# Kernel optimization log

Hardware: AMD Instinct MI355X
Metric: run time of the kernel (lower is better)

The kernel has to match this reference:

```python
import jax, jax.numpy as jnp
import numpy as np

L, H, D, DH, F, V, S, B, CTX = 6, 12, 768, 64, 3072, 32000, 1024, 2, 1024
EPS = 1e-5


def layernorm(x, scale, bias):
    mu = jnp.mean(x, axis=-1, keepdims=True)
    var = jnp.mean(jnp.square(x - mu), axis=-1, keepdims=True)
    return (x - mu) * jax.lax.rsqrt(var + EPS) * scale + bias


def setup_inputs() -> dict:
    key = jax.random.key(0)
    ks = jax.random.split(key, 16)
    std = 0.02
    res_std = 0.02 * (2 * L) ** (-0.5)
    inp = {
        "X": jax.random.randint(ks[0], (B, S), 0, V),
        "emb": jax.random.normal(ks[1], (V, D), jnp.float32) * std,            # tied with head weight
        "pos_emb": jax.random.normal(ks[2], (CTX, D), jnp.float32) * 0.01,
        "Wq": jax.random.normal(ks[3], (L, H, D, DH), jnp.float32) * std,
        "bq": jnp.zeros((L, H, DH), jnp.float32),
        "Wk": jax.random.normal(ks[4], (L, H, D, DH), jnp.float32) * std,
        "bk": jnp.zeros((L, H, DH), jnp.float32),
        "Wv": jax.random.normal(ks[5], (L, H, D, DH), jnp.float32) * std,
        "bv": jnp.zeros((L, H, DH), jnp.float32),
        "Wo": jax.random.normal(ks[6], (L, H * DH, D), jnp.float32) * res_std,  # ResidualScaledLinear
        "bo": jnp.zeros((L, D), jnp.float32),
        "ln1_s": jnp.ones((L, D), jnp.float32),
        "ln1_b": jnp.zeros((L, D), jnp.float32),
        "ln2_s": jnp.ones((L, D), jnp.float32),
        "ln2_b": jnp.zeros((L, D), jnp.float32),
        "W1": jax.random.normal(ks[7], (L, D, F), jnp.float32) * std,
        "b1": jnp.zeros((L, F), jnp.float32),
        "W2": jax.random.normal(ks[8], (L, F, D), jnp.float32) * res_std,       # ResidualScaledLinear
        "b2": jnp.zeros((L, D), jnp.float32),
        "lnf_s": jnp.ones((D,), jnp.float32),
        "lnf_b": jnp.zeros((D,), jnp.float32),
        "head_b": jnp.zeros((V,), jnp.float32),
    }
    return inp


def decoder_forward(X, emb, pos_emb, Wq, bq, Wk, bk, Wv, bv, Wo, bo,
                    ln1_s, ln1_b, ln2_s, ln2_b, W1, b1, W2, b2,
                    lnf_s, lnf_b, head_b):
    seq = X.shape[1]
    x = emb[X] + pos_emb[:seq]                      # [B,S,D]
    causal = jnp.tril(jnp.ones((seq, seq), bool))   # tril mask buffer
    scale = 1.0 / jnp.sqrt(jnp.float32(DH))
    for l in range(L):
        xn = layernorm(x, ln1_s[l], ln1_b[l])
        q = jnp.einsum('bsd,hdk->bhsk', xn, Wq[l]) + bq[l][None, :, None, :]
        k = jnp.einsum('bsd,hdk->bhsk', xn, Wk[l]) + bk[l][None, :, None, :]
        v = jnp.einsum('bsd,hdk->bhsk', xn, Wv[l]) + bv[l][None, :, None, :]
        scores = jnp.einsum('bhsk,bhtk->bhst', q, k) * scale
        scores = jnp.where(causal, scores, -jnp.inf)
        attn = jax.nn.softmax(scores, axis=-1)
        out = jnp.einsum('bhst,bhtk->bshk', attn, v).reshape(x.shape[0], seq, H * DH)
        x = x + out @ Wo[l] + bo[l]
        xn2 = layernorm(x, ln2_s[l], ln2_b[l])
        x = x + jax.nn.relu(xn2 @ W1[l] + b1[l]) @ W2[l] + b2[l]
    x = layernorm(x, lnf_s, lnf_b)
    return x @ emb.T + head_b                       # tied head weight


def reference(X, emb, pos_emb, Wq, bq, Wk, bk, Wv, bv, Wo, bo,
              ln1_s, ln1_b, ln2_s, ln2_b, W1, b1, W2, b2,
              lnf_s, lnf_b, head_b):
    return decoder_forward(X, emb, pos_emb, Wq, bq, Wk, bk, Wv, bv, Wo, bo,
                           ln1_s, ln1_b, ln2_s, ln2_b, W1, b1, W2, b2,
                           lnf_s, lnf_b, head_b)
```

## Files before the change

kernel.cpp:

```cpp
#include <hip/hip_runtime.h>
#include <cstdint>
#include <cstddef>

#define CL 6
#define CH 12
#define CD 768
#define CDH 64
#define CF 3072
#define CV 32000
#define CS 1024
#define CB 2
#define CM (CB*CS)
#define CQS 2304

typedef unsigned short u16;
typedef __bf16 bf16x8 __attribute__((ext_vector_type(8)));
typedef float f32x4 __attribute__((ext_vector_type(4)));

__device__ __forceinline__ float bf2f(u16 u) {
  union { unsigned int i; float f; } c; c.i = ((unsigned int)u) << 16; return c.f;
}
__device__ __forceinline__ u16 f2bf(float f) {
  union { float f; unsigned int i; } c; c.f = f;
  unsigned int lsb = (c.i >> 16) & 1u;
  c.i += 0x7fffu + lsb;
  return (u16)(c.i >> 16);
}

__device__ __forceinline__ void gload16(const u16* g, u16* l) {
  __builtin_amdgcn_global_load_lds(
      (const __attribute__((address_space(1))) void*)g,
      (__attribute__((address_space(3))) void*)l, 16, 0, 0);
}

__global__ __launch_bounds__(256) void convert_kernel(
    const float* __restrict__ src, u16* __restrict__ dst, int total)
{
  int idx = blockIdx.x * 256 + threadIdx.x;
  if (idx < total) dst[idx] = f2bf(src[idx]);
}

__global__ __launch_bounds__(256) void embed_kernel(
    const int* __restrict__ X, const float* __restrict__ emb,
    const float* __restrict__ pos, float* __restrict__ x)
{
  int idx = blockIdx.x * 256 + threadIdx.x;
  int m = idx / CD, d = idx - m * CD;
  int s = m & (CS - 1);
  x[idx] = emb[(size_t)X[m] * CD + d] + pos[s * CD + d];
}

__global__ __launch_bounds__(256) void ln_kernel(
    const float* __restrict__ x, const float* __restrict__ gs,
    const float* __restrict__ gb, u16* __restrict__ out)
{
  __shared__ float rs[4], rss[4];
  int row = blockIdx.x, tid = threadIdx.x;
  const float* xr = x + (size_t)row * CD;
  float a0 = xr[tid], a1 = xr[tid + 256], a2 = xr[tid + 512];
  float s = a0 + a1 + a2;
  float ss = a0 * a0 + a1 * a1 + a2 * a2;
#pragma unroll
  for (int sh = 32; sh > 0; sh >>= 1) {
    s  += __shfl_xor(s, sh, 64);
    ss += __shfl_xor(ss, sh, 64);
  }
  int w = tid >> 6;
  if ((tid & 63) == 0) { rs[w] = s; rss[w] = ss; }
  __syncthreads();
  s  = rs[0] + rs[1] + rs[2] + rs[3];
  ss = rss[0] + rss[1] + rss[2] + rss[3];
  float mu = s * (1.f / CD);
  float inv = rsqrtf(ss * (1.f / CD) - mu * mu + 1e-5f);
  u16* orow = out + (size_t)row * CD;
  orow[tid]       = f2bf((a0 - mu) * inv * gs[tid]       + gb[tid]);
  orow[tid + 256] = f2bf((a1 - mu) * inv * gs[tid + 256] + gb[tid + 256]);
  orow[tid + 512] = f2bf((a2 - mu) * inv * gs[tid + 512] + gb[tid + 512]);
}

__global__ __launch_bounds__(256) void trans_kernel(
    u16* __restrict__ dst, const float* __restrict__ src, int R, int C,
    int PB, long dstL)
{
  __shared__ float st[32][65];
  int r0 = blockIdx.x * 64, c0 = blockIdx.y * 32, bz = blockIdx.z;
  const float* s = src + (size_t)bz * R * C;
  u16* d = dst + (size_t)(bz / PB) * dstL + (size_t)(bz % PB) * R * C;
  int tx = threadIdx.x & 31, ty = threadIdx.x >> 5;
#pragma unroll
  for (int i = 0; i < 8; i++) {
    int r = ty + 8 * i;
    st[tx][r] = s[(size_t)(r0 + r) * C + c0 + tx];
  }
  __syncthreads();
  int j = threadIdx.x & 15, cbase = threadIdx.x >> 4;
#pragma unroll
  for (int i = 0; i < 2; i++) {
    int c = cbase + 16 * i;
    uint2 pk;
    u16* p = (u16*)&pk;
    p[0] = f2bf(st[c][4 * j + 0]);
    p[1] = f2bf(st[c][4 * j + 1]);
    p[2] = f2bf(st[c][4 * j + 2]);
    p[3] = f2bf(st[c][4 * j + 3]);
    *(uint2*)&d[(size_t)(c0 + c) * R + r0 + 4 * j] = pk;
  }
}

__global__ __launch_bounds__(256) void biaspack_kernel(
    const float* __restrict__ bq, const float* __restrict__ bk,
    const float* __restrict__ bv, float* __restrict__ dst)
{
  int idx = blockIdx.x * 256 + threadIdx.x;
  int l = idx / CQS, c = idx - l * CQS;
  float val;
  if (c < 768)       val = bq[l * 768 + c];
  else if (c < 1536) val = bk[l * 768 + c - 768];
  else               val = bv[l * 768 + c - 1536];
  dst[idx] = val;
}

template<bool RES, bool RELU, bool OUTBF>
__global__ __launch_bounds__(256) void gemm64v2_kernel(
    const u16* __restrict__ A, const u16* __restrict__ Bt,
    const float* __restrict__ bias, const float* __restrict__ res,
    void* __restrict__ outp, int M, int N, int K)
{
  __shared__ __align__(16) u16 As[64 * 64];
  __shared__ __align__(16) u16 Bs[64 * 64];
  int tid = threadIdx.x;
  int m0 = blockIdx.y * 64, n0 = blockIdx.x * 64;
  int wv = tid >> 6, ln = tid & 63;
  int quad = ln >> 4, l16 = ln & 15;
  int wm = (wv >> 1) * 32, wn = (wv & 1) * 32;

  int srow = wv * 8 + (ln >> 3);
  int scol = (ln & 7) * 8;
  const u16* gA = A  + (size_t)(m0 + srow) * K + scol;
  const u16* gB = Bt + (size_t)(n0 + srow) * K + scol;

  f32x4 acc[2][2];
  acc[0][0] = f32x4{0,0,0,0}; acc[0][1] = f32x4{0,0,0,0};
  acc[1][0] = f32x4{0,0,0,0}; acc[1][1] = f32x4{0,0,0,0};

  for (int kt = 0; kt < K; kt += 64) {
    __syncthreads();
#pragma unroll
    for (int it = 0; it < 2; it++) {
      gload16(gA + (size_t)it * 32 * K + kt, As + it * 2048 + wv * 512);
      gload16(gB + (size_t)it * 32 * K + kt, Bs + it * 2048 + wv * 512);
    }
    __syncthreads();
#pragma unroll
    for (int h = 0; h < 2; h++) {
      bf16x8 af[2], bf[2];
#pragma unroll
      for (int i = 0; i < 2; i++) {
        af[i] = *reinterpret_cast<const bf16x8*>(&As[(wm + i * 16 + l16) * 64 + h * 32 + quad * 8]);
        bf[i] = *reinterpret_cast<const bf16x8*>(&Bs[(wn + i * 16 + l16) * 64 + h * 32 + quad * 8]);
      }
#pragma unroll
      for (int i = 0; i < 2; i++)
#pragma unroll
        for (int j = 0; j < 2; j++)
          acc[i][j] = __builtin_amdgcn_mfma_f32_16x16x32_bf16(af[i], bf[j], acc[i][j], 0, 0, 0);
    }
  }

#pragma unroll
  for (int i = 0; i < 2; i++) {
    int gmb = m0 + wm + i * 16 + quad * 4;
#pragma unroll
    for (int j = 0; j < 2; j++) {
      int gn = n0 + wn + j * 16 + l16;
      float bsv = bias[gn];
#pragma unroll
      for (int rr = 0; rr < 4; rr++) {
        float val = acc[i][j][rr] + bsv;
        if (RELU) val = fmaxf(val, 0.f);
        size_t o = (size_t)(gmb + rr) * N + gn;
        if (RES) val += res[o];
        if (OUTBF) ((u16*)outp)[o] = f2bf(val);
        else       ((float*)outp)[o] = val;
      }
    }
  }
}

template<bool RES, bool RELU, bool OUTBF>
__global__ __launch_bounds__(256) void gemm128_kernel(
    const u16* __restrict__ A, const u16* __restrict__ Bt,
    const float* __restrict__ bias, const float* __restrict__ res,
    void* __restrict__ outp, int M, int N, int K)
{
  __shared__ __align__(16) u16 As[128 * 64];
  __shared__ __align__(16) u16 Bs[128 * 64];
  int tid = threadIdx.x;
  int nbm = M >> 7, nbn = N >> 7, nwg = nbm * nbn;
  int orig = blockIdx.x;
  int q8 = nwg >> 3, r8 = nwg & 7;
  int xcd = orig & 7;
  int t = ((xcd < r8) ? xcd * (q8 + 1) : r8 * (q8 + 1) + (xcd - r8) * q8) + (orig >> 3);
  int bm = t % nbm, bn = t / nbm;
  int m0 = bm << 7, n0 = bn << 7;

  int wv = tid >> 6, ln = tid & 63;
  int quad = ln >> 4, l16 = ln & 15;
  int wr = wv >> 1, wc = wv & 1;

  int srow = wv * 8 + (ln >> 3);
  int scol = (ln & 7) * 8;
  const u16* gA = A  + (size_t)(m0 + srow) * K + scol;
  const u16* gB = Bt + (size_t)(n0 + srow) * K + scol;

  f32x4 acc[4][4];
#pragma unroll
  for (int i = 0; i < 4; i++)
#pragma unroll
    for (int j = 0; j < 4; j++) acc[i][j] = f32x4{0.f, 0.f, 0.f, 0.f};

  for (int kt = 0; kt < K; kt += 64) {
    __syncthreads();
#pragma unroll
    for (int it = 0; it < 4; it++) {
      gload16(gA + (size_t)it * 32 * K + kt, As + it * 2048 + wv * 512);
      gload16(gB + (size_t)it * 32 * K + kt, Bs + it * 2048 + wv * 512);
    }
    __syncthreads();
#pragma unroll
    for (int h = 0; h < 2; h++) {
      bf16x8 af[4], bf[4];
#pragma unroll
      for (int i = 0; i < 4; i++)
        af[i] = *reinterpret_cast<const bf16x8*>(&As[(wr * 64 + i * 16 + l16) * 64 + h * 32 + quad * 8]);
#pragma unroll
      for (int j = 0; j < 4; j++)
        bf[j] = *reinterpret_cast<const bf16x8*>(&Bs[(wc * 64 + j * 16 + l16) * 64 + h * 32 + quad * 8]);
#pragma unroll
      for (int i = 0; i < 4; i++)
#pragma unroll
        for (int j = 0; j < 4; j++)
          acc[i][j] = __builtin_amdgcn_mfma_f32_16x16x32_bf16(af[i], bf[j], acc[i][j], 0, 0, 0);
    }
  }

#pragma unroll
  for (int i = 0; i < 4; i++) {
    int gm = m0 + wr * 64 + i * 16 + quad * 4;
#pragma unroll
    for (int j = 0; j < 4; j++) {
      int gn = n0 + wc * 64 + j * 16 + l16;
      float bsv = bias[gn];
#pragma unroll
      for (int rr = 0; rr < 4; rr++) {
        float val = acc[i][j][rr] + bsv;
        if (RELU) val = fmaxf(val, 0.f);
        size_t oo = (size_t)(gm + rr) * N + gn;
        if (RES) val += res[oo];
        if (OUTBF) ((u16*)outp)[oo] = f2bf(val);
        else       ((float*)outp)[oo] = val;
      }
    }
  }
}

__global__ __launch_bounds__(256) void attn_mfma_kernel(
    const u16* __restrict__ qkv, u16* __restrict__ o)
{
  __shared__ __align__(16) u16 Ks[64 * 64];
  __shared__ __align__(16) u16 Vt[64 * 64];
  __shared__ __align__(16) u16 Ps[4 * 16 * 64];

  int tid = threadIdx.x;
  int qb = (CS / 64 - 1) - blockIdx.x;
  int h = blockIdx.y, b = blockIdx.z;
  int wid = tid >> 6, lane = tid & 63, quad = lane >> 4, l16 = lane & 15;
  int q0 = qb * 64;
  size_t bh = (size_t)b * CS * CQS + h * CDH;

  bf16x8 aq[2];
  {
    const u16* qrow = qkv + bh + (size_t)(q0 + wid * 16 + l16) * CQS;
#pragma unroll
    for (int ks = 0; ks < 2; ks++) {
      uint4 t = *(const uint4*)(qrow + ks * 32 + quad * 8);
      aq[ks] = *reinterpret_cast<bf16x8*>(&t);
    }
  }

  f32x4 oacc[4];
  float mrow[4], lrow[4];
#pragma unroll
  for (int j = 0; j < 4; j++) oacc[j] = f32x4{0.f, 0.f, 0.f, 0.f};
#pragma unroll
  for (int r = 0; r < 4; r++) { mrow[r] = -1e30f; lrow[r] = 0.f; }

  int srow = tid >> 3, schunk = tid & 7;
  int vrow = tid >> 2, vseg = (tid & 3) * 16;

  for (int t0 = 0; t0 <= q0; t0 += 64) {
    __syncthreads();
#pragma unroll
    for (int it = 0; it < 2; it++) {
      int row = srow + it * 32;
      uint4 kv4 = *(const uint4*)(qkv + bh + 768 + (size_t)(t0 + row) * CQS + schunk * 8);
      *(uint4*)&Ks[row * 64 + ((schunk ^ (row & 7)) * 8)] = kv4;
    }
    {
      const u16* vr = qkv + bh + 1536 + (size_t)(t0 + vrow) * CQS + vseg;
      uint4 a0 = *(const uint4*)(vr);
      uint4 a1 = *(const uint4*)(vr + 8);
      int c = vrow >> 3, w7 = vrow & 7;
#pragma unroll
      for (int i = 0; i < 16; i++) {
        int d = vseg + i;
        u16 val = (i < 8) ? ((const u16*)&a0)[i] : ((const u16*)&a1)[i - 8];
        Vt[d * 64 + (((c ^ (d & 7)) * 8) | w7)] = val;
      }
    }
    __syncthreads();

    f32x4 sacc[4];
#pragma unroll
    for (int j = 0; j < 4; j++) sacc[j] = f32x4{0.f, 0.f, 0.f, 0.f};
#pragma unroll
    for (int j = 0; j < 4; j++) {
      int row = j * 16 + l16;
#pragma unroll
      for (int ks = 0; ks < 2; ks++) {
        bf16x8 bk = *reinterpret_cast<const bf16x8*>(
            &Ks[row * 64 + ((((ks * 4 + quad) ^ (row & 7)) * 8))]);
        sacc[j] = __builtin_amdgcn_mfma_f32_16x16x32_bf16(aq[ks], bk, sacc[j], 0, 0, 0);
      }
    }

    int qg0 = q0 + wid * 16 + quad * 4;
#pragma unroll
    for (int j = 0; j < 4; j++) {
      int tg = t0 + j * 16 + l16;
#pragma unroll
      for (int r = 0; r < 4; r++) {
        float s = sacc[j][r] * 0.125f;
        sacc[j][r] = (tg <= qg0 + r) ? s : -1e30f;
      }
    }

#pragma unroll
    for (int r = 0; r < 4; r++) {
      float m = fmaxf(fmaxf(sacc[0][r], sacc[1][r]), fmaxf(sacc[2][r], sacc[3][r]));
#pragma unroll
      for (int sh = 1; sh < 16; sh <<= 1) m = fmaxf(m, __shfl_xor(m, sh, 64));
      float mnew = fmaxf(mrow[r], m);
      float scal = __expf(mrow[r] - mnew);
      mrow[r] = mnew;
      lrow[r] *= scal;
#pragma unroll
      for (int j = 0; j < 4; j++) oacc[j][r] *= scal;
      float sum = 0.f;
#pragma unroll
      for (int j = 0; j < 4; j++) {
        float p = __expf(sacc[j][r] - mnew);
        sacc[j][r] = p;
        sum += p;
      }
#pragma unroll
      for (int sh = 1; sh < 16; sh <<= 1) sum += __shfl_xor(sum, sh, 64);
      lrow[r] += sum;
    }

    u16* Pw = Ps + wid * 1024;
#pragma unroll
    for (int j = 0; j < 4; j++) {
      int c = (l16 >> 3) + 2 * j;
#pragma unroll
      for (int r = 0; r < 4; r++) {
        int row = quad * 4 + r;
        Pw[row * 64 + (((c ^ (row & 7)) * 8) | (l16 & 7))] = f2bf(sacc[j][r]);
      }
    }

    bf16x8 ap[2];
#pragma unroll
    for (int ks = 0; ks < 2; ks++)
      ap[ks] = *reinterpret_cast<const bf16x8*>(
          &Pw[l16 * 64 + ((((ks * 4 + quad) ^ (l16 & 7)) * 8))]);
#pragma unroll
    for (int j = 0; j < 4; j++) {
      int row = j * 16 + l16;
#pragma unroll
      for (int ks = 0; ks < 2; ks++) {
        bf16x8 bv = *reinterpret_cast<const bf16x8*>(
            &Vt[row * 64 + ((((ks * 4 + quad) ^ (row & 7)) * 8))]);
        oacc[j] = __builtin_amdgcn_mfma_f32_16x16x32_bf16(ap[ks], bv, oacc[j], 0, 0, 0);
      }
    }
  }

#pragma unroll
  for (int r = 0; r < 4; r++) {
    float inv = 1.f / lrow[r];
    int qg = q0 + wid * 16 + quad * 4 + r;
    u16* orow = o + (size_t)b * CS * CD + h * CDH + (size_t)qg * CD;
#pragma unroll
    for (int j = 0; j < 4; j++)
      orow[j * 16 + l16] = f2bf(oacc[j][r] * inv);
  }
}

extern "C" void kernel_launch(void* const* d_in, const int* in_sizes, int n_in,
                              void* d_out, int out_size, void* d_ws, size_t ws_size,
                              hipStream_t stream) {
  const int*   X      = (const int*)d_in[0];
  const float* emb    = (const float*)d_in[1];
  const float* pos    = (const float*)d_in[2];
  const float* Wq     = (const float*)d_in[3];
  const float* bq     = (const float*)d_in[4];
  const float* Wk     = (const float*)d_in[5];
  const float* bk     = (const float*)d_in[6];
  const float* Wv     = (const float*)d_in[7];
  const float* bv     = (const float*)d_in[8];
  const float* Wo     = (const float*)d_in[9];
  const float* bo     = (const float*)d_in[10];
  const float* ln1s   = (const float*)d_in[11];
  const float* ln1b   = (const float*)d_in[12];
  const float* ln2s   = (const float*)d_in[13];
  const float* ln2b   = (const float*)d_in[14];
  const float* W1     = (const float*)d_in[15];
  const float* b1     = (const float*)d_in[16];
  const float* W2     = (const float*)d_in[17];
  const float* b2     = (const float*)d_in[18];
  const float* lnfs   = (const float*)d_in[19];
  const float* lnfb   = (const float*)d_in[20];
  const float* headb  = (const float*)d_in[21];
  (void)in_sizes; (void)n_in; (void)out_size;

  char* ws = (char*)d_ws;
  size_t off = 0;
  auto alloc = [&](size_t bytes) { void* p = ws + off; off += (bytes + 255) & ~(size_t)255; return p; };

  float* x     = (float*)alloc((size_t)CM * CD * 4);
  u16*   xn    = (u16*)  alloc((size_t)CM * CD * 2);
  u16*   qkvb  = (u16*)  alloc((size_t)CM * CQS * 2);
  u16*   ao    = (u16*)  alloc((size_t)CM * CD * 2);
  u16*   hb    = (u16*)  alloc((size_t)CM * CF * 2);
  u16*   embC  = (u16*)  alloc((size_t)CV * CD * 2);
  float* biasp = (float*)alloc((size_t)CL * CQS * 4);

  const size_t WQKV = (size_t)CQS * CD;
  const size_t WOO  = (size_t)CD * CD;
  const size_t WFF  = (size_t)CD * CF;
  size_t perLayerElems = WQKV + WOO + 2 * WFF;
  bool fused = (ws_size >= off + (size_t)CL * perLayerElems * 2 + 4096);
  int LW = fused ? CL : 1;
  u16* Wqkvt = (u16*)alloc((size_t)LW * WQKV * 2);
  u16* Wot   = (u16*)alloc((size_t)LW * WOO * 2);
  u16* W1t   = (u16*)alloc((size_t)LW * WFF * 2);
  u16* W2t   = (u16*)alloc((size_t)LW * WFF * 2);

  embed_kernel<<<CM * CD / 256, 256, 0, stream>>>(X, emb, pos, x);
  convert_kernel<<<(CV * CD) / 256, 256, 0, stream>>>(emb, embC, CV * CD);
  biaspack_kernel<<<(CL * CQS) / 256, 256, 0, stream>>>(bq, bk, bv, biasp);

  if (fused) {
    trans_kernel<<<dim3(CD / 64, CDH / 32, CL * CH), 256, 0, stream>>>(Wqkvt,              Wq, CD, CDH, CH, (long)WQKV);
    trans_kernel<<<dim3(CD / 64, CDH / 32, CL * CH), 256, 0, stream>>>(Wqkvt + 768 * 768,  Wk, CD, CDH, CH, (long)WQKV);
    trans_kernel<<<dim3(CD / 64, CDH / 32, CL * CH), 256, 0, stream>>>(Wqkvt + 1536 * 768, Wv, CD, CDH, CH, (long)WQKV);
    trans_kernel<<<dim3(CD / 64, CD / 32, CL), 256, 0, stream>>>(Wot, Wo, CD, CD, 1, (long)WOO);
    trans_kernel<<<dim3(CD / 64, CF / 32, CL), 256, 0, stream>>>(W1t, W1, CD, CF, 1, (long)WFF);
    trans_kernel<<<dim3(CF / 64, CD / 32, CL), 256, 0, stream>>>(W2t, W2, CF, CD, 1, (long)WFF);
  }

  const int QKV_TOT = CH * CD * CDH;

  for (int l = 0; l < CL; l++) {
    if (!fused) {
      trans_kernel<<<dim3(CD / 64, CDH / 32, CH), 256, 0, stream>>>(Wqkvt,              Wq + (size_t)l * QKV_TOT, CD, CDH, CH, (long)WQKV);
      trans_kernel<<<dim3(CD / 64, CDH / 32, CH), 256, 0, stream>>>(Wqkvt + 768 * 768,  Wk + (size_t)l * QKV_TOT, CD, CDH, CH, (long)WQKV);
      trans_kernel<<<dim3(CD / 64, CDH / 32, CH), 256, 0, stream>>>(Wqkvt + 1536 * 768, Wv + (size_t)l * QKV_TOT, CD, CDH, CH, (long)WQKV);
      trans_kernel<<<dim3(CD / 64, CD / 32, 1), 256, 0, stream>>>(Wot, Wo + (size_t)l * WOO, CD, CD, 1, (long)WOO);
      trans_kernel<<<dim3(CD / 64, CF / 32, 1), 256, 0, stream>>>(W1t, W1 + (size_t)l * WFF, CD, CF, 1, (long)WFF);
      trans_kernel<<<dim3(CF / 64, CD / 32, 1), 256, 0, stream>>>(W2t, W2 + (size_t)l * WFF, CF, CD, 1, (long)WFF);
    }
    int lw = fused ? l : 0;
    const u16* wqkv = Wqkvt + (size_t)lw * WQKV;
    const u16* wot  = Wot   + (size_t)lw * WOO;
    const u16* w1t  = W1t   + (size_t)lw * WFF;
    const u16* w2t  = W2t   + (size_t)lw * WFF;

    ln_kernel<<<CM, 256, 0, stream>>>(x, ln1s + l * CD, ln1b + l * CD, xn);

    gemm128_kernel<false, false, true><<<(CM / 128) * (CQS / 128), 256, 0, stream>>>(
        xn, wqkv, biasp + l * CQS, nullptr, qkvb, CM, CQS, CD);

    attn_mfma_kernel<<<dim3(CS / 64, CH, CB), 256, 0, stream>>>(qkvb, ao);

    gemm64v2_kernel<true, false, false><<<dim3(CD / 64, CM / 64), 256, 0, stream>>>(
        ao, wot, bo + l * CD, x, x, CM, CD, CD);

    ln_kernel<<<CM, 256, 0, stream>>>(x, ln2s + l * CD, ln2b + l * CD, xn);

    gemm128_kernel<false, true, true><<<(CM / 128) * (CF / 128), 256, 0, stream>>>(
        xn, w1t, b1 + l * CF, nullptr, hb, CM, CF, CD);

    gemm64v2_kernel<true, false, false><<<dim3(CD / 64, CM / 64), 256, 0, stream>>>(
        hb, w2t, b2 + l * CD, x, x, CM, CD, CF);
  }

  ln_kernel<<<CM, 256, 0, stream>>>(x, lnfs, lnfb, xn);
  gemm128_kernel<false, false, false><<<(CM / 128) * (CV / 128), 256, 0, stream>>>(
      xn, embC, headb, nullptr, d_out, CM, CV, CD);
}
```

Before: 1.579 ms.

## Double-buffer K/V tiles in attention and shrink GEMM K-tile to 32

The attention kernel now double-buffers K and V tiles in shared memory. It prefetches the next K tile through direct global-to-LDS loads and the next V tile into registers, transposing V after the compute, so one barrier per iteration is removed and loads overlap the MFMA work. Both GEMM kernels switch from a 64-wide to a 32-wide K tile, which halves LDS use per block and may raise occupancy. The cost is twice as many barrier-separated iterations, with no prefetch in the GEMMs.

```diff
diff --git a/kernel.cpp b/kernel.cpp
--- a/kernel.cpp
+++ b/kernel.cpp
@@ -121,50 +121,44 @@
 }
 
 template<bool RES, bool RELU, bool OUTBF>
-__global__ __launch_bounds__(256) void gemm64v2_kernel(
+__global__ __launch_bounds__(256) void gemm64v3_kernel(
     const u16* __restrict__ A, const u16* __restrict__ Bt,
     const float* __restrict__ bias, const float* __restrict__ res,
     void* __restrict__ outp, int M, int N, int K)
 {
-  __shared__ __align__(16) u16 As[64 * 64];
-  __shared__ __align__(16) u16 Bs[64 * 64];
+  __shared__ __align__(16) u16 As[64 * 32];
+  __shared__ __align__(16) u16 Bs[64 * 32];
   int tid = threadIdx.x;
   int m0 = blockIdx.y * 64, n0 = blockIdx.x * 64;
   int wv = tid >> 6, ln = tid & 63;
   int quad = ln >> 4, l16 = ln & 15;
   int wm = (wv >> 1) * 32, wn = (wv & 1) * 32;
-
-  int srow = wv * 8 + (ln >> 3);
-  int scol = (ln & 7) * 8;
+  int srow = tid >> 2, scol = (tid & 3) * 8;
   const u16* gA = A  + (size_t)(m0 + srow) * K + scol;
   const u16* gB = Bt + (size_t)(n0 + srow) * K + scol;
+  u16* lA = As + wv * 512;
+  u16* lB = Bs + wv * 512;
 
   f32x4 acc[2][2];
   acc[0][0] = f32x4{0,0,0,0}; acc[0][1] = f32x4{0,0,0,0};
   acc[1][0] = f32x4{0,0,0,0}; acc[1][1] = f32x4{0,0,0,0};
 
-  for (int kt = 0; kt < K; kt += 64) {
+  for (int kt = 0; kt < K; kt += 32) {
     __syncthreads();
-#pragma unroll
-    for (int it = 0; it < 2; it++) {
-      gload16(gA + (size_t)it * 32 * K + kt, As + it * 2048 + wv * 512);
-      gload16(gB + (size_t)it * 32 * K + kt, Bs + it * 2048 + wv * 512);
-    }
+    gload16(gA + kt, lA);
+    gload16(gB + kt, lB);
     __syncthreads();
-#pragma unroll
-    for (int h = 0; h < 2; h++) {
-      bf16x8 af[2], bf[2];
-#pragma unroll
-      for (int i = 0; i < 2; i++) {
-        af[i] = *reinterpret_cast<const bf16x8*>(&As[(wm + i * 16 + l16) * 64 + h * 32 + quad * 8]);
-        bf[i] = *reinterpret_cast<const bf16x8*>(&Bs[(wn + i * 16 + l16) * 64 + h * 32 + quad * 8]);
-      }
-#pragma unroll
-      for (int i = 0; i < 2; i++)
-#pragma unroll
-        for (int j = 0; j < 2; j++)
-          acc[i][j] = __builtin_amdgcn_mfma_f32_16x16x32_bf16(af[i], bf[j], acc[i][j], 0, 0, 0);
-    }
+    bf16x8 af[2], bfr[2];
+#pragma unroll
+    for (int i = 0; i < 2; i++) {
+      af[i]  = *reinterpret_cast<const bf16x8*>(&As[(wm + i * 16 + l16) * 32 + quad * 8]);
+      bfr[i] = *reinterpret_cast<const bf16x8*>(&Bs[(wn + i * 16 + l16) * 32 + quad * 8]);
+    }
+#pragma unroll
+    for (int i = 0; i < 2; i++)
+#pragma unroll
+      for (int j = 0; j < 2; j++)
+        acc[i][j] = __builtin_amdgcn_mfma_f32_16x16x32_bf16(af[i], bfr[j], acc[i][j], 0, 0, 0);
   }
 
 #pragma unroll
@@ -193,8 +187,8 @@
     const float* __restrict__ bias, const float* __restrict__ res,
     void* __restrict__ outp, int M, int N, int K)
 {
-  __shared__ __align__(16) u16 As[128 * 64];
-  __shared__ __align__(16) u16 Bs[128 * 64];
+  __shared__ __align__(16) u16 As[128 * 32];
+  __shared__ __align__(16) u16 Bs[128 * 32];
   int tid = threadIdx.x;
   int nbm = M >> 7, nbn = N >> 7, nwg = nbm * nbn;
   int orig = blockIdx.x;
@@ -208,10 +202,16 @@
   int quad = ln >> 4, l16 = ln & 15;
   int wr = wv >> 1, wc = wv & 1;
 
-  int srow = wv * 8 + (ln >> 3);
-  int scol = (ln & 7) * 8;
-  const u16* gA = A  + (size_t)(m0 + srow) * K + scol;
-  const u16* gB = Bt + (size_t)(n0 + srow) * K + scol;
+  int srow = wv * 16 + (ln >> 2);
+  int scol = (ln & 3) * 8;
+  const u16* ga0 = A  + (size_t)(m0 + srow) * K + scol;
+  const u16* ga1 = A  + (size_t)(m0 + srow + 64) * K + scol;
+  const u16* gb0 = Bt + (size_t)(n0 + srow) * K + scol;
+  const u16* gb1 = Bt + (size_t)(n0 + srow + 64) * K + scol;
+  u16* lA0 = As + wv * 512;
+  u16* lA1 = As + 2048 + wv * 512;
+  u16* lB0 = Bs + wv * 512;
+  u16* lB1 = Bs + 2048 + wv * 512;
 
   f32x4 acc[4][4];
 #pragma unroll
@@ -219,29 +219,25 @@
 #pragma unroll
     for (int j = 0; j < 4; j++) acc[i][j] = f32x4{0.f, 0.f, 0.f, 0.f};
 
-  for (int kt = 0; kt < K; kt += 64) {
+  for (int kt = 0; kt < K; kt += 32) {
     __syncthreads();
-#pragma unroll
-    for (int it = 0; it < 4; it++) {
-      gload16(gA + (size_t)it * 32 * K + kt, As + it * 2048 + wv * 512);
-      gload16(gB + (size_t)it * 32 * K + kt, Bs + it * 2048 + wv * 512);
-    }
+    gload16(ga0 + kt, lA0);
+    gload16(ga1 + kt, lA1);
+    gload16(gb0 + kt, lB0);
+    gload16(gb1 + kt, lB1);
     __syncthreads();
-#pragma unroll
-    for (int h = 0; h < 2; h++) {
-      bf16x8 af[4], bf[4];
-#pragma unroll
-      for (int i = 0; i < 4; i++)
-        af[i] = *reinterpret_cast<const bf16x8*>(&As[(wr * 64 + i * 16 + l16) * 64 + h * 32 + quad * 8]);
+    bf16x8 af[4], bf[4];
+#pragma unroll
+    for (int i = 0; i < 4; i++)
+      af[i] = *reinterpret_cast<const bf16x8*>(&As[(wr * 64 + i * 16 + l16) * 32 + quad * 8]);
+#pragma unroll
+    for (int j = 0; j < 4; j++)
+      bf[j] = *reinterpret_cast<const bf16x8*>(&Bs[(wc * 64 + j * 16 + l16) * 32 + quad * 8]);
+#pragma unroll
+    for (int i = 0; i < 4; i++)
 #pragma unroll
       for (int j = 0; j < 4; j++)
-        bf[j] = *reinterpret_cast<const bf16x8*>(&Bs[(wc * 64 + j * 16 + l16) * 64 + h * 32 + quad * 8]);
-#pragma unroll
-      for (int i = 0; i < 4; i++)
-#pragma unroll
-        for (int j = 0; j < 4; j++)
-          acc[i][j] = __builtin_amdgcn_mfma_f32_16x16x32_bf16(af[i], bf[j], acc[i][j], 0, 0, 0);
-    }
+        acc[i][j] = __builtin_amdgcn_mfma_f32_16x16x32_bf16(af[i], bf[j], acc[i][j], 0, 0, 0);
   }
 
 #pragma unroll
@@ -267,8 +263,8 @@
 __global__ __launch_bounds__(256) void attn_mfma_kernel(
     const u16* __restrict__ qkv, u16* __restrict__ o)
 {
-  __shared__ __align__(16) u16 Ks[64 * 64];
-  __shared__ __align__(16) u16 Vt[64 * 64];
+  __shared__ __align__(16) u16 Ks[2][64 * 64];
+  __shared__ __align__(16) u16 Vt[2][64 * 64];
   __shared__ __align__(16) u16 Ps[4 * 16 * 64];
 
   int tid = threadIdx.x;
@@ -278,6 +274,11 @@
   int q0 = qb * 64;
   size_t bh = (size_t)b * CS * CQS + h * CDH;
 
+  const u16* kbase = qkv + bh + 768;
+  const u16* vbase = qkv + bh + 1536;
+
+  int t4 = (tid & 15) * 4, dg = (tid >> 4) * 4;
+
   bf16x8 aq[2];
   {
     const u16* qrow = qkv + bh + (size_t)(q0 + wid * 16 + l16) * CQS;
@@ -295,30 +296,48 @@
 #pragma unroll
   for (int r = 0; r < 4; r++) { mrow[r] = -1e30f; lrow[r] = 0.f; }
 
-  int srow = tid >> 3, schunk = tid & 7;
-  int vrow = tid >> 2, vseg = (tid & 3) * 16;
+  {
+#pragma unroll
+    for (int it = 0; it < 2; it++) {
+      int c = it * 256 + tid;
+      int row = c >> 3, c8l = c & 7;
+      gload16(kbase + (size_t)row * CQS + (((c8l ^ (row & 7)) * 8)),
+              &Ks[0][(it * 256 + wid * 64) * 8]);
+    }
+    uint2 vr[4];
+#pragma unroll
+    for (int i = 0; i < 4; i++)
+      vr[i] = *(const uint2*)(vbase + (size_t)(t4 + i) * CQS + dg);
+#pragma unroll
+    for (int j = 0; j < 4; j++) {
+      int d = dg + j;
+      uint2 pk;
+      u16* p = (u16*)&pk;
+      p[0] = ((const u16*)&vr[0])[j]; p[1] = ((const u16*)&vr[1])[j];
+      p[2] = ((const u16*)&vr[2])[j]; p[3] = ((const u16*)&vr[3])[j];
+      *(uint2*)&Vt[0][d * 64 + (((t4 >> 3) ^ (d & 7)) * 8) + (t4 & 4)] = pk;
+    }
+  }
 
   for (int t0 = 0; t0 <= q0; t0 += 64) {
+    int cur = (t0 >> 6) & 1;
     __syncthreads();
-#pragma unroll
-    for (int it = 0; it < 2; it++) {
-      int row = srow + it * 32;
-      uint4 kv4 = *(const uint4*)(qkv + bh + 768 + (size_t)(t0 + row) * CQS + schunk * 8);
-      *(uint4*)&Ks[row * 64 + ((schunk ^ (row & 7)) * 8)] = kv4;
-    }
-    {
-      const u16* vr = qkv + bh + 1536 + (size_t)(t0 + vrow) * CQS + vseg;
-      uint4 a0 = *(const uint4*)(vr);
-      uint4 a1 = *(const uint4*)(vr + 8);
-      int c = vrow >> 3, w7 = vrow & 7;
-#pragma unroll
-      for (int i = 0; i < 16; i++) {
-        int d = vseg + i;
-        u16 val = (i < 8) ? ((const u16*)&a0)[i] : ((const u16*)&a1)[i - 8];
-        Vt[d * 64 + (((c ^ (d & 7)) * 8) | w7)] = val;
-      }
-    }
-    __syncthreads();
+    bool hasnext = (t0 + 64 <= q0);
+    uint2 vr[4];
+    if (hasnext) {
+      const u16* vb2 = vbase + (size_t)(t0 + 64) * CQS;
+#pragma unroll
+      for (int i = 0; i < 4; i++)
+        vr[i] = *(const uint2*)(vb2 + (size_t)(t4 + i) * CQS + dg);
+      const u16* kb2 = kbase + (size_t)(t0 + 64) * CQS;
+#pragma unroll
+      for (int it = 0; it < 2; it++) {
+        int c = it * 256 + tid;
+        int row = c >> 3, c8l = c & 7;
+        gload16(kb2 + (size_t)row * CQS + (((c8l ^ (row & 7)) * 8)),
+                &Ks[cur ^ 1][(it * 256 + wid * 64) * 8]);
+      }
+    }
 
     f32x4 sacc[4];
 #pragma unroll
@@ -329,7 +348,7 @@
 #pragma unroll
       for (int ks = 0; ks < 2; ks++) {
         bf16x8 bk = *reinterpret_cast<const bf16x8*>(
-            &Ks[row * 64 + ((((ks * 4 + quad) ^ (row & 7)) * 8))]);
+            &Ks[cur][row * 64 + ((((ks * 4 + quad) ^ (row & 7)) * 8))]);
         sacc[j] = __builtin_amdgcn_mfma_f32_16x16x32_bf16(aq[ks], bk, sacc[j], 0, 0, 0);
       }
     }
@@ -390,8 +409,20 @@
 #pragma unroll
       for (int ks = 0; ks < 2; ks++) {
         bf16x8 bv = *reinterpret_cast<const bf16x8*>(
-            &Vt[row * 64 + ((((ks * 4 + quad) ^ (row & 7)) * 8))]);
+            &Vt[cur][row * 64 + ((((ks * 4 + quad) ^ (row & 7)) * 8))]);
         oacc[j] = __builtin_amdgcn_mfma_f32_16x16x32_bf16(ap[ks], bv, oacc[j], 0, 0, 0);
+      }
+    }
+
+    if (hasnext) {
+#pragma unroll
+      for (int j = 0; j < 4; j++) {
+        int d = dg + j;
+        uint2 pk;
+        u16* p = (u16*)&pk;
+        p[0] = ((const u16*)&vr[0])[j]; p[1] = ((const u16*)&vr[1])[j];
+        p[2] = ((const u16*)&vr[2])[j]; p[3] = ((const u16*)&vr[3])[j];
+        *(uint2*)&Vt[cur ^ 1][d * 64 + (((t4 >> 3) ^ (d & 7)) * 8) + (t4 & 4)] = pk;
       }
     }
   }
@@ -494,7 +525,7 @@
 
     attn_mfma_kernel<<<dim3(CS / 64, CH, CB), 256, 0, stream>>>(qkvb, ao);
 
-    gemm64v2_kernel<true, false, false><<<dim3(CD / 64, CM / 64), 256, 0, stream>>>(
+    gemm64v3_kernel<true, false, false><<<dim3(CD / 64, CM / 64), 256, 0, stream>>>(
         ao, wot, bo + l * CD, x, x, CM, CD, CD);
 
     ln_kernel<<<CM, 256, 0, stream>>>(x, ln2s + l * CD, ln2b + l * CD, xn);
@@ -502,7 +533,7 @@
     gemm128_kernel<false, true, true><<<(CM / 128) * (CF / 128), 256, 0, stream>>>(
         xn, w1t, b1 + l * CF, nullptr, hb, CM, CF, CD);
 
-    gemm64v2_kernel<true, false, false><<<dim3(CD / 64, CM / 64), 256, 0, stream>>>(
+    gemm64v3_kernel<true, false, false><<<dim3(CD / 64, CM / 64), 256, 0, stream>>>(
         hb, w2t, b2 + l * CD, x, x, CM, CD, CF);
   }
 
```

Result: no change. 1.570 ms (-0.6%).
